# Kernel tuning notes

Measured on AMD Instinct MI355X. Metric: run time of the kernel, lower is better.

Reference implementation:

```python
import jax, jax.numpy as jnp
import numpy as np

N_NODES = 50000
N_EDGES = 500000
N_GRAPHS = 100
D = 146
N_CLASSES = 10
BN_EPS = 1e-5


def setup_inputs() -> dict:
    key = jax.random.key(0)
    ks = jax.random.split(key, 16)
    nodes_feat = jax.random.normal(ks[0], (N_NODES, D), dtype=jnp.float32)
    src = jax.random.randint(ks[1], (N_EDGES,), 0, N_NODES)
    dst = jax.random.randint(ks[2], (N_EDGES,), 0, N_NODES)
    graph_ids = jnp.sort(jax.random.randint(ks[3], (N_NODES,), 0, N_GRAPHS))
    # snorm_n = 1/sqrt(num_nodes of the graph each node belongs to)
    counts = jax.ops.segment_sum(jnp.ones((N_NODES,), jnp.float32), graph_ids, N_GRAPHS)
    counts = jnp.maximum(counts, 1.0)
    snorm_n = (1.0 / jnp.sqrt(counts))[graph_ids][:, None]
    s = 1.0 / np.sqrt(D)
    W_emb = jax.random.uniform(ks[4], (D, D), jnp.float32, -s, s)
    b_emb = jnp.zeros((D,), jnp.float32)
    # 4 stacked GCN layers (gcn_1, gcn_2, gcn_3, gcn_o)
    Ws = jax.random.uniform(ks[5], (4, D, D), jnp.float32, -s, s)
    bs = jnp.zeros((4, D), jnp.float32)
    gammas = jnp.ones((4, D), jnp.float32)
    betas = jnp.zeros((4, D), jnp.float32)
    # MLPReadout: 146 -> 73 -> 36 -> 10
    h1, h2 = D // 2, D // 4
    W_r0 = jax.random.uniform(ks[6], (D, h1), jnp.float32, -s, s)
    b_r0 = jnp.zeros((h1,), jnp.float32)
    W_r1 = jax.random.uniform(ks[7], (h1, h2), jnp.float32, -1/np.sqrt(h1), 1/np.sqrt(h1))
    b_r1 = jnp.zeros((h2,), jnp.float32)
    W_r2 = jax.random.uniform(ks[8], (h2, N_CLASSES), jnp.float32, -1/np.sqrt(h2), 1/np.sqrt(h2))
    b_r2 = jnp.zeros((N_CLASSES,), jnp.float32)
    return {"nodes_feat": nodes_feat, "snorm_n": snorm_n, "W_emb": W_emb, "b_emb": b_emb,
            "Ws": Ws, "bs": bs, "gammas": gammas, "betas": betas,
            "W_r0": W_r0, "b_r0": b_r0, "W_r1": W_r1, "b_r1": b_r1, "W_r2": W_r2, "b_r2": b_r2,
            "src": src, "dst": dst, "graph_ids": graph_ids}


def _degree_norms(src, dst):
    ones = jnp.ones((src.shape[0],), jnp.float32)
    deg_out = jnp.maximum(jax.ops.segment_sum(ones, src, N_NODES), 1.0)
    deg_in = jnp.maximum(jax.ops.segment_sum(ones, dst, N_NODES), 1.0)
    return jax.lax.rsqrt(deg_out), jax.lax.rsqrt(deg_in)


def _gcn_layer(h, W, b, gamma, beta, snorm_n, src, dst, norm_src, norm_dst):
    # DGL GraphConv(norm='both'): out = D_in^-1/2 * A^T * (D_out^-1/2 * (h W)) + b
    h_in = h
    hW = (h * norm_src[:, None]) @ W                      # [N, D]
    msg = hW[src]                                          # gather [E, D]
    agg = jax.ops.segment_sum(msg, dst, N_NODES)           # scatter-add [N, D]
    h = agg * norm_dst[:, None] + b
    h = h * snorm_n                                        # graph size norm
    # BatchNorm1d, training-mode batch statistics over nodes
    mean = jnp.mean(h, axis=0)
    var = jnp.var(h, axis=0)
    h = (h - mean) * jax.lax.rsqrt(var + BN_EPS) * gamma + beta
    h = jax.nn.relu(h)
    return h_in + h                                        # residual


def _mean_nodes(h, graph_ids):
    counts = jnp.maximum(jax.ops.segment_sum(jnp.ones((N_NODES,), h.dtype), graph_ids, N_GRAPHS), 1.0)
    return jax.ops.segment_sum(h, graph_ids, N_GRAPHS) / counts[:, None]


def reference(nodes_feat, snorm_n, W_emb, b_emb, Ws, bs, gammas, betas,
              W_r0, b_r0, W_r1, b_r1, W_r2, b_r2, src, dst, graph_ids):
    norm_src, norm_dst = _degree_norms(src, dst)
    h = nodes_feat @ W_emb + b_emb
    hg = jnp.zeros((N_GRAPHS, D), h.dtype)
    for i in range(4):
        h = _gcn_layer(h, Ws[i], bs[i], gammas[i], betas[i], snorm_n, src, dst, norm_src, norm_dst)
        hg = hg + _mean_nodes(h, graph_ids)
    # MLPReadout
    z = jax.nn.relu(hg @ W_r0 + b_r0)
    z = jax.nn.relu(z @ W_r1 + b_r1)
    return z @ W_r2 + b_r2
```

## Files before the change

kernel.cpp:

```cpp
#include <hip/hip_runtime.h>
#include <hip/hip_fp16.h>

#define D 146
#define AS 160
#define HWS 80
#define NG 100
#define BN_EPS 1e-5f

typedef _Float16 half8 __attribute__((ext_vector_type(8)));
typedef float f32x4 __attribute__((ext_vector_type(4)));

__global__ void packw_k(const float* __restrict__ Wemb, const float* __restrict__ Ws,
                        __half* __restrict__ Wf)
{
    int idx = blockIdx.x * 256 + threadIdx.x;
    if (idx >= 5 * 5 * 10 * 64 * 8) return;
    int i8 = idx & 7;
    int l  = (idx >> 3) & 63;
    int t  = (idx >> 9) % 10;
    int s  = (idx / (8 * 64 * 10)) % 5;
    int m  = idx / (8 * 64 * 10 * 5);
    int k = s * 32 + ((l >> 4) << 3) + i8;
    int c = t * 16 + (l & 15);
    float v = 0.0f;
    if (k < D && c < D) {
        const float* Wsrc = (m == 0) ? Wemb : (Ws + (size_t)(m - 1) * D * D);
        v = Wsrc[k * D + c];
    }
    Wf[idx] = __float2half(v);
}

__global__ void cvtnodes_k(const float* __restrict__ nodes, __half2* __restrict__ out2, int N)
{
    int idx = blockIdx.x * 256 + threadIdx.x;
    if (idx >= N * HWS) return;
    int r = idx / HWS, j = idx % HWS;
    int c = 2 * j;
    float v0 = (c < D) ? nodes[(size_t)r * D + c] : 0.0f;
    float v1 = (c + 1 < D) ? nodes[(size_t)r * D + c + 1] : 0.0f;
    out2[idx] = __floats2half2_rn(v0, v1);
}

__global__ void deg_k(const int* __restrict__ src, const int* __restrict__ dst,
                      int* __restrict__ co, int* __restrict__ ci, int E)
{
    int e = blockIdx.x * 256 + threadIdx.x;
    if (e >= E) return;
    atomicAdd(&co[src[e]], 1);
    atomicAdd(&ci[dst[e]], 1);
}

__global__ void rsq_k(const int* __restrict__ co, const int* __restrict__ ci,
                      float* __restrict__ ns, float* __restrict__ nd, int N)
{
    int i = blockIdx.x * 256 + threadIdx.x;
    if (i >= N) return;
    ns[i] = rsqrtf(fmaxf((float)co[i], 1.0f));
    nd[i] = rsqrtf(fmaxf((float)ci[i], 1.0f));
}

__global__ __launch_bounds__(256) void pscan1_k(const int* __restrict__ cnt,
                                                int* __restrict__ bsum, int N)
{
    __shared__ int lds[256];
    int t = blockIdx.x * 256 + threadIdx.x;
    lds[threadIdx.x] = (t < N) ? ((cnt[t] + 7) & ~7) : 0;
    __syncthreads();
    for (int s = 128; s > 0; s >>= 1) {
        if (threadIdx.x < s) lds[threadIdx.x] += lds[threadIdx.x + s];
        __syncthreads();
    }
    if (threadIdx.x == 0) bsum[blockIdx.x] = lds[0];
}

__global__ __launch_bounds__(256) void pscan2_k(const int* __restrict__ bsum,
                                                int* __restrict__ boff, int nb)
{
    __shared__ int lds[256];
    int t = threadIdx.x;
    int v = (t < nb) ? bsum[t] : 0;
    lds[t] = v;
    __syncthreads();
    for (int off = 1; off < 256; off <<= 1) {
        int u = (t >= off) ? lds[t - off] : 0;
        __syncthreads();
        lds[t] += u;
        __syncthreads();
    }
    boff[t] = lds[t] - v;
}

__global__ __launch_bounds__(256) void pscan3_k(const int* __restrict__ cnt,
                                                const int* __restrict__ boff,
                                                int* __restrict__ rowptr,
                                                int* __restrict__ cursor, int N)
{
    __shared__ int lds[256];
    int t = blockIdx.x * 256 + threadIdx.x;
    int v = (t < N) ? ((cnt[t] + 7) & ~7) : 0;
    lds[threadIdx.x] = v;
    __syncthreads();
    for (int off = 1; off < 256; off <<= 1) {
        int u = (threadIdx.x >= off) ? lds[threadIdx.x - off] : 0;
        __syncthreads();
        lds[threadIdx.x] += u;
        __syncthreads();
    }
    if (t < N) {
        int r = boff[blockIdx.x] + lds[threadIdx.x] - v;
        rowptr[t] = r;
        cursor[t] = r;
    }
}

__global__ void rowend_k(const int* __restrict__ cnt, const int* __restrict__ rowptr,
                         int* __restrict__ rowptrN, int N)
{
    if (threadIdx.x == 0 && blockIdx.x == 0)
        rowptrN[0] = rowptr[N - 1] + ((cnt[N - 1] + 7) & ~7);
}

__global__ void padfill_k(const int* __restrict__ cnt, const int* __restrict__ rowptr,
                          int* __restrict__ esrc, int N)
{
    int n = blockIdx.x * 256 + threadIdx.x;
    if (n >= N) return;
    int b = rowptr[n] + cnt[n];
    int ee = rowptr[n] + ((cnt[n] + 7) & ~7);
    for (int i = b; i < ee; ++i) esrc[i] = N;
}

__global__ void csrfill_k(const int* __restrict__ src, const int* __restrict__ dst,
                          int* __restrict__ cursor, int* __restrict__ esrc, int E)
{
    int e = blockIdx.x * 256 + threadIdx.x;
    if (e >= E) return;
    int pos = atomicAdd(&cursor[dst[e]], 1);
    esrc[pos] = src[e];
}

__global__ void part_k(const int* __restrict__ rowptr, int* __restrict__ wstart,
                       int N, int NW)
{
    int w = blockIdx.x * 256 + threadIdx.x;
    if (w > NW) return;
    if (w == NW) { wstart[NW] = N; return; }
    if (w == 0) { wstart[0] = 0; return; }
    long long Epad = rowptr[N];
    long long target = Epad * w / NW;
    int lo = 0, hi = N;
    while (lo < hi) {
        int mid = (lo + hi) >> 1;
        if ((long long)rowptr[mid] <= target) lo = mid + 1; else hi = mid;
    }
    wstart[w] = lo - 1;
}

__global__ __launch_bounds__(256) void gemm_mfma(
    const __half* __restrict__ A16, const __half* __restrict__ Wf,
    __half* __restrict__ C16h, __half* __restrict__ H16, int nrows,
    const float* __restrict__ rowscale, const float* __restrict__ bias)
{
    int lane = threadIdx.x & 63, wave = threadIdx.x >> 6;
    int m0 = blockIdx.x * 128 + wave * 32;
    int ar0 = min(m0 + (lane & 15), nrows - 1);
    int ar1 = min(m0 + 16 + (lane & 15), nrows - 1);
    int ak = (lane >> 4) * 8;

    f32x4 acc0[10] = {};
    f32x4 acc1[10] = {};
    const half8* WfV = reinterpret_cast<const half8*>(Wf);
#pragma unroll
    for (int s = 0; s < 5; ++s) {
        half8 a0 = *reinterpret_cast<const half8*>(&A16[(size_t)ar0 * AS + s * 32 + ak]);
        half8 a1 = *reinterpret_cast<const half8*>(&A16[(size_t)ar1 * AS + s * 32 + ak]);
        const half8* wrow = WfV + (size_t)(s * 10) * 64 + lane;
#pragma unroll
        for (int t = 0; t < 10; ++t) {
            half8 b = wrow[(size_t)t * 64];
            acc0[t] = __builtin_amdgcn_mfma_f32_16x16x32_f16(a0, b, acc0[t], 0, 0, 0);
            acc1[t] = __builtin_amdgcn_mfma_f32_16x16x32_f16(a1, b, acc1[t], 0, 0, 0);
        }
    }

    int ccol = lane & 15;
    {
        int rbase = m0 + (lane >> 4) * 4;
        if (H16) {
            float rsv[4];
#pragma unroll
            for (int j = 0; j < 4; ++j) {
                int r = rbase + j;
                rsv[j] = (r < nrows) ? rowscale[r] : 0.0f;
            }
#pragma unroll
            for (int t = 0; t < 10; ++t) {
                int c = t * 16 + ccol;
                float bv = (c < D) ? bias[c] : 0.0f;
#pragma unroll
                for (int j = 0; j < 4; ++j) {
                    int r = rbase + j;
                    if (r >= nrows) continue;
                    float v = acc0[t][j] + bv;
                    H16[(size_t)r * AS + c] = __float2half(v);
                    C16h[(size_t)r * AS + c] = __float2half(v * rsv[j]);
                }
            }
        } else {
#pragma unroll
            for (int t = 0; t < 10; ++t) {
                int c = t * 16 + ccol;
                if (c >= D) continue;
#pragma unroll
                for (int j = 0; j < 4; ++j) {
                    int r = rbase + j;
                    if (r >= nrows) continue;
                    C16h[(size_t)r * AS + c] = __float2half(acc0[t][j]);
                }
            }
        }
    }
    {
        int rbase = m0 + 16 + (lane >> 4) * 4;
        if (H16) {
            float rsv[4];
#pragma unroll
            for (int j = 0; j < 4; ++j) {
                int r = rbase + j;
                rsv[j] = (r < nrows) ? rowscale[r] : 0.0f;
            }
#pragma unroll
            for (int t = 0; t < 10; ++t) {
                int c = t * 16 + ccol;
                float bv = (c < D) ? bias[c] : 0.0f;
#pragma unroll
                for (int j = 0; j < 4; ++j) {
                    int r = rbase + j;
                    if (r >= nrows) continue;
                    float v = acc1[t][j] + bv;
                    H16[(size_t)r * AS + c] = __float2half(v);
                    C16h[(size_t)r * AS + c] = __float2half(v * rsv[j]);
                }
            }
        } else {
#pragma unroll
            for (int t = 0; t < 10; ++t) {
                int c = t * 16 + ccol;
                if (c >= D) continue;
#pragma unroll
                for (int j = 0; j < 4; ++j) {
                    int r = rbase + j;
                    if (r >= nrows) continue;
                    C16h[(size_t)r * AS + c] = __float2half(acc1[t][j]);
                }
            }
        }
    }
}

__global__ __launch_bounds__(256) void agg_k(
    const __half2* __restrict__ hW2, const int* __restrict__ esrc,
    const int* __restrict__ rowptr, const int* __restrict__ wstart,
    const float* __restrict__ nd, const float* __restrict__ sn,
    const float* __restrict__ bias,
    __half2* __restrict__ hpre2, float* __restrict__ stats, int N)
{
    __shared__ float rs[4][D];
    __shared__ float rq[4][D];
    int lane = threadIdx.x & 63, wave = threadIdx.x >> 6;
    int w = blockIdx.x * 4 + wave;
    int w0 = wstart[w], w1 = wstart[w + 1];

    bool v1 = lane < 9;
    int j0 = lane, j1 = 64 + lane;
    int c0 = 2 * lane, c1 = 128 + 2 * lane;
    int c1m = v1 ? c1 : 0;
    float b00 = bias[c0], b01 = bias[c0 + 1];
    float b10 = bias[c1m], b11 = bias[c1m + 1];
    float s00 = 0, s01 = 0, s10 = 0, s11 = 0, q00 = 0, q01 = 0, q10 = 0, q11 = 0;

    int e = (w0 < w1) ? rowptr[w0] : 0;
    for (int n = w0; n < w1; ++n) {
        int ee = rowptr[n + 1];
        float a00 = 0, a01 = 0, a10 = 0, a11 = 0;
        for (; e < ee; e += 8) {
            int4 i0 = *reinterpret_cast<const int4*>(&esrc[e]);
            int4 i1 = *reinterpret_cast<const int4*>(&esrc[e + 4]);
            const __half2* p0 = hW2 + (size_t)i0.x * HWS;
            const __half2* p1 = hW2 + (size_t)i0.y * HWS;
            const __half2* p2 = hW2 + (size_t)i0.z * HWS;
            const __half2* p3 = hW2 + (size_t)i0.w * HWS;
            const __half2* p4 = hW2 + (size_t)i1.x * HWS;
            const __half2* p5 = hW2 + (size_t)i1.y * HWS;
            const __half2* p6 = hW2 + (size_t)i1.z * HWS;
            const __half2* p7 = hW2 + (size_t)i1.w * HWS;
            float2 f0 = __half22float2(p0[j0]);
            float2 f1 = __half22float2(p1[j0]);
            float2 f2 = __half22float2(p2[j0]);
            float2 f3 = __half22float2(p3[j0]);
            float2 f4 = __half22float2(p4[j0]);
            float2 f5 = __half22float2(p5[j0]);
            float2 f6 = __half22float2(p6[j0]);
            float2 f7 = __half22float2(p7[j0]);
            a00 += ((f0.x + f1.x) + (f2.x + f3.x)) + ((f4.x + f5.x) + (f6.x + f7.x));
            a01 += ((f0.y + f1.y) + (f2.y + f3.y)) + ((f4.y + f5.y) + (f6.y + f7.y));
            if (v1) {
                float2 g0 = __half22float2(p0[j1]);
                float2 g1 = __half22float2(p1[j1]);
                float2 g2 = __half22float2(p2[j1]);
                float2 g3 = __half22float2(p3[j1]);
                float2 g4 = __half22float2(p4[j1]);
                float2 g5 = __half22float2(p5[j1]);
                float2 g6 = __half22float2(p6[j1]);
                float2 g7 = __half22float2(p7[j1]);
                a10 += ((g0.x + g1.x) + (g2.x + g3.x)) + ((g4.x + g5.x) + (g6.x + g7.x));
                a11 += ((g0.y + g1.y) + (g2.y + g3.y)) + ((g4.y + g5.y) + (g6.y + g7.y));
            }
        }
        float ndv = nd[n], snv = sn[n];
        float h00 = (a00 * ndv + b00) * snv;
        float h01 = (a01 * ndv + b01) * snv;
        hpre2[(size_t)n * (D / 2) + j0] = __floats2half2_rn(h00, h01);
        s00 += h00; q00 = fmaf(h00, h00, q00);
        s01 += h01; q01 = fmaf(h01, h01, q01);
        if (v1) {
            float h10 = (a10 * ndv + b10) * snv;
            float h11 = (a11 * ndv + b11) * snv;
            hpre2[(size_t)n * (D / 2) + j1] = __floats2half2_rn(h10, h11);
            s10 += h10; q10 = fmaf(h10, h10, q10);
            s11 += h11; q11 = fmaf(h11, h11, q11);
        }
    }
    rs[wave][c0] = s00; rs[wave][c0 + 1] = s01;
    rq[wave][c0] = q00; rq[wave][c0 + 1] = q01;
    if (v1) {
        rs[wave][c1] = s10; rs[wave][c1 + 1] = s11;
        rq[wave][c1] = q10; rq[wave][c1 + 1] = q11;
    }
    __syncthreads();
    for (int cc = threadIdx.x; cc < D; cc += 256) {
        atomicAdd(&stats[cc], rs[0][cc] + rs[1][cc] + rs[2][cc] + rs[3][cc]);
        atomicAdd(&stats[D + cc], rq[0][cc] + rq[1][cc] + rq[2][cc] + rq[3][cc]);
    }
}

__global__ __launch_bounds__(256) void p2hg_k(
    __half2* __restrict__ h2, const __half2* __restrict__ hpre2,
    const float* __restrict__ stats, const float* __restrict__ gamma,
    const float* __restrict__ beta, const float* __restrict__ sn,
    const float* __restrict__ nsrc, const int* __restrict__ gid,
    __half2* __restrict__ hs2, float* __restrict__ hg, int N)
{
    int lane = threadIdx.x & 63, wave = threadIdx.x >> 6;
    int per = (N + gridDim.x - 1) / gridDim.x;
    int n0 = blockIdx.x * per;
    int n1 = min(N, n0 + per);
    int wper = (per + 3) >> 2;
    int w0 = min(n1, n0 + wave * wper);
    int w1 = min(n1, w0 + wper);
    if (w0 >= w1) return;

    bool v1 = lane < 9;
    bool wr = (hs2 != nullptr);
    int j0 = lane, j1 = 64 + lane;
    int c0 = 2 * lane, c1 = 128 + 2 * lane;
    int c1m = v1 ? c1 : 0;
    float inv = 1.0f / (float)N;
    float m00 = stats[c0] * inv,     m01 = stats[c0 + 1] * inv;
    float m10 = stats[c1m] * inv,    m11 = stats[c1m + 1] * inv;
    float v00 = fmaxf(stats[D + c0] * inv - m00 * m00, 0.0f);
    float v01 = fmaxf(stats[D + c0 + 1] * inv - m01 * m01, 0.0f);
    float v10 = fmaxf(stats[D + c1m] * inv - m10 * m10, 0.0f);
    float v11 = fmaxf(stats[D + c1m + 1] * inv - m11 * m11, 0.0f);
    float r00 = rsqrtf(v00 + BN_EPS), r01 = rsqrtf(v01 + BN_EPS);
    float r10 = rsqrtf(v10 + BN_EPS), r11 = rsqrtf(v11 + BN_EPS);
    float g00 = gamma[c0], g01 = gamma[c0 + 1], t00 = beta[c0], t01 = beta[c0 + 1];
    float g10 = gamma[c1m], g11 = gamma[c1m + 1], t10 = beta[c1m], t11 = beta[c1m + 1];

    int g = gid[w0];
    float a00 = 0, a01 = 0, a10 = 0, a11 = 0;
    for (int n = w0; n < w1; ++n) {
        int gr = gid[n];
        if (gr != g) {
            atomicAdd(&hg[(size_t)g * D + c0], a00);
            atomicAdd(&hg[(size_t)g * D + c0 + 1], a01);
            if (v1) {
                atomicAdd(&hg[(size_t)g * D + c1], a10);
                atomicAdd(&hg[(size_t)g * D + c1 + 1], a11);
            }
            a00 = a01 = a10 = a11 = 0;
            g = gr;
        }
        float ns = nsrc[n];
        float w2 = sn[n]; w2 *= w2;
        float2 hv = __half22float2(h2[(size_t)n * HWS + j0]);
        float2 p0 = __half22float2(hpre2[(size_t)n * (D / 2) + j0]);
        float x0 = hv.x + fmaxf((p0.x - m00) * r00 * g00 + t00, 0.0f);
        float x1 = hv.y + fmaxf((p0.y - m01) * r01 * g01 + t01, 0.0f);
        if (wr) {
            h2[(size_t)n * HWS + j0] = __floats2half2_rn(x0, x1);
            hs2[(size_t)n * HWS + j0] = __floats2half2_rn(x0 * ns, x1 * ns);
        }
        a00 = fmaf(x0, w2, a00);
        a01 = fmaf(x1, w2, a01);
        if (v1) {
            float2 hv1 = __half22float2(h2[(size_t)n * HWS + j1]);
            float2 p1 = __half22float2(hpre2[(size_t)n * (D / 2) + j1]);
            float x2 = hv1.x + fmaxf((p1.x - m10) * r10 * g10 + t10, 0.0f);
            float x3 = hv1.y + fmaxf((p1.y - m11) * r11 * g11 + t11, 0.0f);
            if (wr) {
                h2[(size_t)n * HWS + j1] = __floats2half2_rn(x2, x3);
                hs2[(size_t)n * HWS + j1] = __floats2half2_rn(x2 * ns, x3 * ns);
            }
            a10 = fmaf(x2, w2, a10);
            a11 = fmaf(x3, w2, a11);
        }
    }
    atomicAdd(&hg[(size_t)g * D + c0], a00);
    atomicAdd(&hg[(size_t)g * D + c0 + 1], a01);
    if (v1) {
        atomicAdd(&hg[(size_t)g * D + c1], a10);
        atomicAdd(&hg[(size_t)g * D + c1 + 1], a11);
    }
}

__global__ __launch_bounds__(128) void readout_k(
    const float* __restrict__ hg,
    const float* __restrict__ W0, const float* __restrict__ b0,
    const float* __restrict__ W1, const float* __restrict__ b1,
    const float* __restrict__ W2, const float* __restrict__ b2,
    float* __restrict__ out)
{
    __shared__ float hl[D];
    __shared__ float z1[73];
    __shared__ float z2[36];
    int g = blockIdx.x;
    int t = threadIdx.x;
    for (int i = t; i < D; i += 128) hl[i] = hg[(size_t)g * D + i];
    __syncthreads();
    if (t < 73) {
        float s = b0[t];
        for (int k = 0; k < D; ++k) s = fmaf(hl[k], W0[k * 73 + t], s);
        z1[t] = fmaxf(s, 0.0f);
    }
    __syncthreads();
    if (t < 36) {
        float s = b1[t];
        for (int k = 0; k < 73; ++k) s = fmaf(z1[k], W1[k * 36 + t], s);
        z2[t] = fmaxf(s, 0.0f);
    }
    __syncthreads();
    if (t < 10) {
        float s = b2[t];
        for (int k = 0; k < 36; ++k) s = fmaf(z2[k], W2[k * 10 + t], s);
        out[g * 10 + t] = s;
    }
}

extern "C" void kernel_launch(void* const* d_in, const int* in_sizes, int n_in,
                              void* d_out, int out_size, void* d_ws, size_t ws_size,
                              hipStream_t stream)
{
    const float* nodes  = (const float*)d_in[0];
    const float* snorm  = (const float*)d_in[1];
    const float* Wemb   = (const float*)d_in[2];
    const float* bemb   = (const float*)d_in[3];
    const float* Ws     = (const float*)d_in[4];
    const float* bs     = (const float*)d_in[5];
    const float* gammas = (const float*)d_in[6];
    const float* betas  = (const float*)d_in[7];
    const float* Wr0    = (const float*)d_in[8];
    const float* br0    = (const float*)d_in[9];
    const float* Wr1    = (const float*)d_in[10];
    const float* br1    = (const float*)d_in[11];
    const float* Wr2    = (const float*)d_in[12];
    const float* br2    = (const float*)d_in[13];
    const int*   src    = (const int*)d_in[14];
    const int*   dst    = (const int*)d_in[15];
    const int*   gid    = (const int*)d_in[16];

    int N = in_sizes[0] / D;
    int E = in_sizes[14];
    int nb = (N + 255) / 256;
    const int NWF = 5 * 5 * 10 * 64 * 8;
    int Ecap = E + 8 * ((N + 7) & ~7);
    const int AGB = 1024;
    const int NW = AGB * 4;

    float* ws = (float*)d_ws;
    size_t off = 0;
    float* nsrc  = ws + off; off += N;
    float* ndst  = ws + off; off += N;
    float* stats = ws + off; off += 4 * 4 * D;
    float* hg    = ws + off; off += (size_t)NG * D;
    int* cnt_out = (int*)(ws + off); off += N;
    int* cnt_in  = (int*)(ws + off); off += N;
    int* rowptr  = (int*)(ws + off); off += N + 4;
    int* cursor  = (int*)(ws + off); off += N;
    int* esrc    = (int*)(ws + off); off += Ecap;
    int* bsum    = (int*)(ws + off); off += 256;
    int* boff    = (int*)(ws + off); off += 256;
    int* wstart  = (int*)(ws + off); off += NW + 4;
    off = (off + 3) & ~(size_t)3;
    __half* Wf      = (__half*)(ws + off); off += NWF / 2;
    __half* h16     = (__half*)(ws + off); off += (size_t)N * AS / 2;
    __half* hs16    = (__half*)(ws + off); off += (size_t)N * AS / 2;
    __half* nodes16 = (__half*)(ws + off);
    __half* hW16    = (__half*)(ws + off); off += (size_t)(N + 1) * AS / 2;
    __half* hpre16  = (__half*)(ws + off); off += (size_t)N * D / 2;

    hipMemsetAsync(cnt_out, 0, 2 * (size_t)N * sizeof(int), stream);
    hipMemsetAsync(stats, 0, (16 * D + (size_t)NG * D) * sizeof(float), stream);
    hipMemsetAsync(hW16 + (size_t)N * AS, 0, AS * sizeof(__half), stream);
    packw_k<<<(NWF + 255) / 256, 256, 0, stream>>>(Wemb, Ws, Wf);
    cvtnodes_k<<<(N * HWS + 255) / 256, 256, 0, stream>>>(nodes, (__half2*)nodes16, N);
    deg_k<<<(E + 255) / 256, 256, 0, stream>>>(src, dst, cnt_out, cnt_in, E);
    rsq_k<<<(N + 255) / 256, 256, 0, stream>>>(cnt_out, cnt_in, nsrc, ndst, N);
    pscan1_k<<<nb, 256, 0, stream>>>(cnt_in, bsum, N);
    pscan2_k<<<1, 256, 0, stream>>>(bsum, boff, nb);
    pscan3_k<<<nb, 256, 0, stream>>>(cnt_in, boff, rowptr, cursor, N);
    rowend_k<<<1, 64, 0, stream>>>(cnt_in, rowptr, rowptr + N, N);
    padfill_k<<<nb, 256, 0, stream>>>(cnt_in, rowptr, esrc, N);
    csrfill_k<<<(E + 255) / 256, 256, 0, stream>>>(src, dst, cursor, esrc, E);
    part_k<<<(NW + 256) / 256, 256, 0, stream>>>(rowptr, wstart, N, NW);

    int gblk = (N + 127) / 128;
    gemm_mfma<<<gblk, 256, 0, stream>>>(nodes16, Wf, hs16, h16, N, nsrc, bemb);

    for (int l = 0; l < 4; ++l) {
        float* st = stats + (size_t)l * 4 * D;
        gemm_mfma<<<gblk, 256, 0, stream>>>(hs16, Wf + (size_t)(l + 1) * (NWF / 5),
                                            hW16, nullptr, N, nullptr, nullptr);
        agg_k<<<AGB, 256, 0, stream>>>((const __half2*)hW16, esrc, rowptr, wstart, ndst, snorm,
                                       bs + (size_t)l * D, (__half2*)hpre16, st, N);
        p2hg_k<<<2048, 256, 0, stream>>>((__half2*)h16, (const __half2*)hpre16, st,
                                         gammas + (size_t)l * D, betas + (size_t)l * D,
                                         snorm, nsrc, gid,
                                         (l == 3) ? nullptr : (__half2*)hs16, hg, N);
    }

    readout_k<<<NG, 128, 0, stream>>>(hg, Wr0, br0, Wr1, br1, Wr2, br2, (float*)d_out);
}
```

Before: 556.5 us.

## Pack GEMM epilogue stores, interleave two nodes in aggregation, merge memsets

The GEMM epilogue now uses a lane shuffle so even lanes write half2 pairs, halving the number of store instructions. The aggregation kernel processes two destination nodes at once, interleaving their gathers to raise memory-level parallelism. The workspace is reordered so a single memset clears the stats, hg and degree counters. These trade extra registers and shuffles for fewer stores and more loads in flight.

```diff
diff --git a/kernel.cpp b/kernel.cpp
--- a/kernel.cpp
+++ b/kernel.cpp
@@ -184,8 +184,11 @@
     }
 
     int ccol = lane & 15;
-    {
-        int rbase = m0 + (lane >> 4) * 4;
+    bool evenl = (lane & 1) == 0;
+#pragma unroll
+    for (int tile = 0; tile < 2; ++tile) {
+        int rbase = m0 + tile * 16 + (lane >> 4) * 4;
+        f32x4* acc = tile ? acc1 : acc0;
         if (H16) {
             float rsv[4];
 #pragma unroll
@@ -200,61 +203,70 @@
 #pragma unroll
                 for (int j = 0; j < 4; ++j) {
                     int r = rbase + j;
-                    if (r >= nrows) continue;
-                    float v = acc0[t][j] + bv;
-                    H16[(size_t)r * AS + c] = __float2half(v);
-                    C16h[(size_t)r * AS + c] = __float2half(v * rsv[j]);
+                    float v = acc[t][j] + bv;
+                    float vn = __shfl_xor(v, 1);
+                    if (evenl && r < nrows) {
+                        *reinterpret_cast<__half2*>(&H16[(size_t)r * AS + c]) =
+                            __floats2half2_rn(v, vn);
+                        *reinterpret_cast<__half2*>(&C16h[(size_t)r * AS + c]) =
+                            __floats2half2_rn(v * rsv[j], vn * rsv[j]);
+                    }
                 }
             }
         } else {
 #pragma unroll
             for (int t = 0; t < 10; ++t) {
                 int c = t * 16 + ccol;
-                if (c >= D) continue;
 #pragma unroll
                 for (int j = 0; j < 4; ++j) {
                     int r = rbase + j;
-                    if (r >= nrows) continue;
-                    C16h[(size_t)r * AS + c] = __float2half(acc0[t][j]);
+                    float v = acc[t][j];
+                    float vn = __shfl_xor(v, 1);
+                    if (evenl && c < D && r < nrows)
+                        *reinterpret_cast<__half2*>(&C16h[(size_t)r * AS + c]) =
+                            __floats2half2_rn(v, vn);
                 }
             }
         }
     }
-    {
-        int rbase = m0 + 16 + (lane >> 4) * 4;
-        if (H16) {
-            float rsv[4];
-#pragma unroll
-            for (int j = 0; j < 4; ++j) {
-                int r = rbase + j;
-                rsv[j] = (r < nrows) ? rowscale[r] : 0.0f;
-            }
-#pragma unroll
-            for (int t = 0; t < 10; ++t) {
-                int c = t * 16 + ccol;
-                float bv = (c < D) ? bias[c] : 0.0f;
-#pragma unroll
-                for (int j = 0; j < 4; ++j) {
-                    int r = rbase + j;
-                    if (r >= nrows) continue;
-                    float v = acc1[t][j] + bv;
-                    H16[(size_t)r * AS + c] = __float2half(v);
-                    C16h[(size_t)r * AS + c] = __float2half(v * rsv[j]);
-                }
-            }
-        } else {
-#pragma unroll
-            for (int t = 0; t < 10; ++t) {
-                int c = t * 16 + ccol;
-                if (c >= D) continue;
-#pragma unroll
-                for (int j = 0; j < 4; ++j) {
-                    int r = rbase + j;
-                    if (r >= nrows) continue;
-                    C16h[(size_t)r * AS + c] = __float2half(acc1[t][j]);
-                }
-            }
-        }
+}
+
+__device__ __forceinline__ void g8(const __half2* __restrict__ hW2,
+                                   const int* __restrict__ esrc, int e,
+                                   int j0, int j1, bool v1,
+                                   float& a00, float& a01, float& a10, float& a11)
+{
+    int4 i0 = *reinterpret_cast<const int4*>(&esrc[e]);
+    int4 i1 = *reinterpret_cast<const int4*>(&esrc[e + 4]);
+    const __half2* p0 = hW2 + (size_t)i0.x * HWS;
+    const __half2* p1 = hW2 + (size_t)i0.y * HWS;
+    const __half2* p2 = hW2 + (size_t)i0.z * HWS;
+    const __half2* p3 = hW2 + (size_t)i0.w * HWS;
+    const __half2* p4 = hW2 + (size_t)i1.x * HWS;
+    const __half2* p5 = hW2 + (size_t)i1.y * HWS;
+    const __half2* p6 = hW2 + (size_t)i1.z * HWS;
+    const __half2* p7 = hW2 + (size_t)i1.w * HWS;
+    float2 f0 = __half22float2(p0[j0]);
+    float2 f1 = __half22float2(p1[j0]);
+    float2 f2 = __half22float2(p2[j0]);
+    float2 f3 = __half22float2(p3[j0]);
+    float2 f4 = __half22float2(p4[j0]);
+    float2 f5 = __half22float2(p5[j0]);
+    float2 f6 = __half22float2(p6[j0]);
+    float2 f7 = __half22float2(p7[j0]);
+    a00 += ((f0.x + f1.x) + (f2.x + f3.x)) + ((f4.x + f5.x) + (f6.x + f7.x));
+    a01 += ((f0.y + f1.y) + (f2.y + f3.y)) + ((f4.y + f5.y) + (f6.y + f7.y));
+    if (v1) {
+        float2 g0 = __half22float2(p0[j1]);
+        float2 g1 = __half22float2(p1[j1]);
+        float2 g2 = __half22float2(p2[j1]);
+        float2 g3 = __half22float2(p3[j1]);
+        float2 g4 = __half22float2(p4[j1]);
+        float2 g5 = __half22float2(p5[j1]);
+        float2 g6 = __half22float2(p6[j1]);
+        float2 g7 = __half22float2(p7[j1]);
+        a10 += ((g0.x + g1.x) + (g2.x + g3.x)) + ((g4.x + g5.x) + (g6.x + g7.x));
+        a11 += ((g0.y + g1.y) + (g2.y + g3.y)) + ((g4.y + g5.y) + (g6.y + g7.y));
     }
 }
 
@@ -279,44 +291,7 @@
     float b10 = bias[c1m], b11 = bias[c1m + 1];
     float s00 = 0, s01 = 0, s10 = 0, s11 = 0, q00 = 0, q01 = 0, q10 = 0, q11 = 0;
 
-    int e = (w0 < w1) ? rowptr[w0] : 0;
-    for (int n = w0; n < w1; ++n) {
-        int ee = rowptr[n + 1];
-        float a00 = 0, a01 = 0, a10 = 0, a11 = 0;
-        for (; e < ee; e += 8) {
-            int4 i0 = *reinterpret_cast<const int4*>(&esrc[e]);
-            int4 i1 = *reinterpret_cast<const int4*>(&esrc[e + 4]);
-            const __half2* p0 = hW2 + (size_t)i0.x * HWS;
-            const __half2* p1 = hW2 + (size_t)i0.y * HWS;
-            const __half2* p2 = hW2 + (size_t)i0.z * HWS;
-            const __half2* p3 = hW2 + (size_t)i0.w * HWS;
-            const __half2* p4 = hW2 + (size_t)i1.x * HWS;
-            const __half2* p5 = hW2 + (size_t)i1.y * HWS;
-            const __half2* p6 = hW2 + (size_t)i1.z * HWS;
-            const __half2* p7 = hW2 + (size_t)i1.w * HWS;
-            float2 f0 = __half22float2(p0[j0]);
-            float2 f1 = __half22float2(p1[j0]);
-            float2 f2 = __half22float2(p2[j0]);
-            float2 f3 = __half22float2(p3[j0]);
-            float2 f4 = __half22float2(p4[j0]);
-            float2 f5 = __half22float2(p5[j0]);
-            float2 f6 = __half22float2(p6[j0]);
-            float2 f7 = __half22float2(p7[j0]);
-            a00 += ((f0.x + f1.x) + (f2.x + f3.x)) + ((f4.x + f5.x) + (f6.x + f7.x));
-            a01 += ((f0.y + f1.y) + (f2.y + f3.y)) + ((f4.y + f5.y) + (f6.y + f7.y));
-            if (v1) {
-                float2 g0 = __half22float2(p0[j1]);
-                float2 g1 = __half22float2(p1[j1]);
-                float2 g2 = __half22float2(p2[j1]);
-                float2 g3 = __half22float2(p3[j1]);
-                float2 g4 = __half22float2(p4[j1]);
-                float2 g5 = __half22float2(p5[j1]);
-                float2 g6 = __half22float2(p6[j1]);
-                float2 g7 = __half22float2(p7[j1]);
-                a10 += ((g0.x + g1.x) + (g2.x + g3.x)) + ((g4.x + g5.x) + (g6.x + g7.x));
-                a11 += ((g0.y + g1.y) + (g2.y + g3.y)) + ((g4.y + g5.y) + (g6.y + g7.y));
-            }
-        }
+    auto finish = [&](int n, float a00, float a01, float a10, float a11) {
         float ndv = nd[n], snv = sn[n];
         float h00 = (a00 * ndv + b00) * snv;
         float h01 = (a01 * ndv + b01) * snv;
@@ -330,7 +305,31 @@
             s10 += h10; q10 = fmaf(h10, h10, q10);
             s11 += h11; q11 = fmaf(h11, h11, q11);
         }
-    }
+    };
+
+    int n = w0;
+    for (; n + 1 < w1; n += 2) {
+        int ea = rowptr[n], eea = rowptr[n + 1];
+        int eb = eea,       eeb = rowptr[n + 2];
+        float A00 = 0, A01 = 0, A10 = 0, A11 = 0;
+        float B00 = 0, B01 = 0, B10 = 0, B11 = 0;
+        while (ea < eea && eb < eeb) {
+            g8(hW2, esrc, ea, j0, j1, v1, A00, A01, A10, A11);
+            g8(hW2, esrc, eb, j0, j1, v1, B00, B01, B10, B11);
+            ea += 8; eb += 8;
+        }
+        for (; ea < eea; ea += 8) g8(hW2, esrc, ea, j0, j1, v1, A00, A01, A10, A11);
+        for (; eb < eeb; eb += 8) g8(hW2, esrc, eb, j0, j1, v1, B00, B01, B10, B11);
+        finish(n, A00, A01, A10, A11);
+        finish(n + 1, B00, B01, B10, B11);
+    }
+    if (n < w1) {
+        int ea = rowptr[n], eea = rowptr[n + 1];
+        float A00 = 0, A01 = 0, A10 = 0, A11 = 0;
+        for (; ea < eea; ea += 8) g8(hW2, esrc, ea, j0, j1, v1, A00, A01, A10, A11);
+        finish(n, A00, A01, A10, A11);
+    }
+
     rs[wave][c0] = s00; rs[wave][c0 + 1] = s01;
     rq[wave][c0] = q00; rq[wave][c0 + 1] = q01;
     if (v1) {
@@ -489,12 +488,13 @@
 
     float* ws = (float*)d_ws;
     size_t off = 0;
-    float* nsrc  = ws + off; off += N;
-    float* ndst  = ws + off; off += N;
     float* stats = ws + off; off += 4 * 4 * D;
     float* hg    = ws + off; off += (size_t)NG * D;
     int* cnt_out = (int*)(ws + off); off += N;
     int* cnt_in  = (int*)(ws + off); off += N;
+    size_t zbytes = (16 * D + (size_t)NG * D + 2 * (size_t)N) * 4;
+    float* nsrc  = ws + off; off += N;
+    float* ndst  = ws + off; off += N;
     int* rowptr  = (int*)(ws + off); off += N + 4;
     int* cursor  = (int*)(ws + off); off += N;
     int* esrc    = (int*)(ws + off); off += Ecap;
@@ -509,8 +509,7 @@
     __half* hW16    = (__half*)(ws + off); off += (size_t)(N + 1) * AS / 2;
     __half* hpre16  = (__half*)(ws + off); off += (size_t)N * D / 2;
 
-    hipMemsetAsync(cnt_out, 0, 2 * (size_t)N * sizeof(int), stream);
-    hipMemsetAsync(stats, 0, (16 * D + (size_t)NG * D) * sizeof(float), stream);
+    hipMemsetAsync(stats, 0, zbytes, stream);
     hipMemsetAsync(hW16 + (size_t)N * AS, 0, AS * sizeof(__half), stream);
     packw_k<<<(NWF + 255) / 256, 256, 0, stream>>>(Wemb, Ws, Wf);
     cvtnodes_k<<<(N * HWS + 255) / 256, 256, 0, stream>>>(nodes, (__half2*)nodes16, N);
```

Result: no change. 552.0 us (-0.8%).
